# Kernel tuning notes

Measured on AMD Instinct MI355X. Metric: run time of the kernel, lower is better.

The kernel has to match this reference:

```python
import jax, jax.numpy as jnp
import numpy as np

N = 10000      # num nodes
D = 256        # embedding dim (in_channels)
Q = 4096       # num query edges
P = 0.003      # edge density (~30 avg degree)


def setup_inputs() -> dict:
    key = jax.random.key(0)
    k1, k2, k3 = jax.random.split(key, 3)
    emb_weight = jax.random.normal(k1, (N, D), dtype=jnp.float32)
    # 0/1 dense adjacency standing in for the SparseTensor adj
    adj = (jax.random.uniform(k2, (N, N)) < P).astype(jnp.float32)
    edges = jax.random.randint(k3, (2, Q), 0, N, dtype=jnp.int64)
    return {"emb_weight": emb_weight, "adj": adj, "edges": edges}


def reference(emb_weight, adj, edges):
    # model_type='simplecos', x=None -> x = emb.weight
    x = emb_weight
    degrees = adj.sum(-1) + 1e-6                      # [N]
    # x = x + (adj @ x) / degrees[:, None]  (torch precedence: matmul then div)
    x = x + (adj @ x) / degrees[:, None]              # [N, D]
    # cosine_similarity with eps=1e-8 (torch default)
    nrm = jnp.sqrt(jnp.sum(x * x, axis=1))            # [N]
    xn = x / jnp.maximum(nrm, 1e-8)[:, None]          # [N, D]
    # common neighbors: elementwise product of adjacency rows of the two endpoints
    src, dst = edges[0], edges[1]
    cn = adj[src] * adj[dst]                          # [Q, N]
    mask = (cn != 0).astype(x.dtype)                  # [Q, N] indicator of common neighbor
    # cos(x[src[e]], x[c]) and cos(x[dst[e]], x[c]) for every candidate neighbor c
    cosL = xn[src] @ xn.T                             # [Q, N]
    cosR = xn[dst] @ xn.T                             # [Q, N]
    # sparse segment-sum over common-neighbor columns
    weights = jnp.sum(mask * cosL * cosR, axis=1)     # [Q]
    return jax.nn.sigmoid(weights)
```

## Files before the change

### kernel.cpp

```cpp
#include <hip/hip_runtime.h>
#include <math.h>

#define NN 10000
#define DD 256
#define QQ 4096
#define CAP 128

typedef float  fx4 __attribute__((ext_vector_type(4)));


__global__ __launch_bounds__(256) void scan_rows(
    const float* __restrict__ adj, int* __restrict__ cnt, int* __restrict__ nbr)
{
    const int i = blockIdx.x;
    const int t = threadIdx.x;
    __shared__ int s_cnt;
    __shared__ int s_list[CAP];
    if (t == 0) s_cnt = 0;
    __syncthreads();

    const fx4* row = (const fx4*)(adj + (size_t)i * NN);
    fx4 r[10];
    #pragma unroll
    for (int j = 0; j < 10; ++j) {
        int k = t + j * 256;
        if (k < NN / 4) r[j] = __builtin_nontemporal_load(&row[k]);
        else            r[j] = (fx4){0.f, 0.f, 0.f, 0.f};
    }
    #pragma unroll
    for (int j = 0; j < 10; ++j) {
        fx4 v = r[j];
        int base = (t + j * 256) * 4;
        if (v.x != 0.f) { int p = atomicAdd(&s_cnt, 1); if (p < CAP) s_list[p] = base;     }
        if (v.y != 0.f) { int p = atomicAdd(&s_cnt, 1); if (p < CAP) s_list[p] = base + 1; }
        if (v.z != 0.f) { int p = atomicAdd(&s_cnt, 1); if (p < CAP) s_list[p] = base + 2; }
        if (v.w != 0.f) { int p = atomicAdd(&s_cnt, 1); if (p < CAP) s_list[p] = base + 3; }
    }
    __syncthreads();

    const int c = s_cnt;
    if (t == 0) cnt[i] = c;
    const int m = (c < CAP) ? c : CAP;
    if (t < m) nbr[(size_t)i * CAP + t] = s_list[t];
}

__global__ __launch_bounds__(256) void gather_rows(
    const float* __restrict__ emb, const int* __restrict__ cnt,
    const int* __restrict__ nbr, float* __restrict__ xn)
{
    const int i = blockIdx.x;
    const int t = threadIdx.x;
    __shared__ int   s_list[CAP];
    __shared__ float s_red[4];
    __shared__ float s_norm;

    const int c = cnt[i];
    const int m = (c < CAP) ? c : CAP;

    const float self = emb[(size_t)i * DD + t];
    if (t < m) s_list[t] = nbr[(size_t)i * CAP + t];
    __syncthreads();

    float a0=0.f,a1=0.f,a2=0.f,a3=0.f,a4=0.f,a5=0.f,a6=0.f,a7=0.f;
    int k = 0;
    for (; k + 8 <= m; k += 8) {
        int i0=s_list[k],   i1=s_list[k+1], i2=s_list[k+2], i3=s_list[k+3];
        int i4=s_list[k+4], i5=s_list[k+5], i6=s_list[k+6], i7=s_list[k+7];
        a0 += emb[(size_t)i0*DD + t]; a1 += emb[(size_t)i1*DD + t];
        a2 += emb[(size_t)i2*DD + t]; a3 += emb[(size_t)i3*DD + t];
        a4 += emb[(size_t)i4*DD + t]; a5 += emb[(size_t)i5*DD + t];
        a6 += emb[(size_t)i6*DD + t]; a7 += emb[(size_t)i7*DD + t];
    }
    for (; k < m; ++k) a0 += emb[(size_t)s_list[k]*DD + t];
    const float acc = ((a0+a1)+(a2+a3)) + ((a4+a5)+(a6+a7));

    const float deg = (float)c + 1e-6f;
    const float x = self + acc / deg;

    float s = x * x;
    #pragma unroll
    for (int o = 32; o > 0; o >>= 1) s += __shfl_down(s, o, 64);
    const int lane = t & 63, wv = t >> 6;
    if (lane == 0) s_red[wv] = s;
    __syncthreads();
    if (t == 0) {
        float tot = s_red[0] + s_red[1] + s_red[2] + s_red[3];
        s_norm = fmaxf(sqrtf(tot), 1e-8f);
    }
    __syncthreads();

    xn[(size_t)i * DD + t] = x / s_norm;
}

__global__ __launch_bounds__(64) void edge_weights(
    const int* __restrict__ edges, const float* __restrict__ xn,
    const int* __restrict__ cnt, const int* __restrict__ nbr,
    float* __restrict__ out)
{
    const int e = blockIdx.x;
    const int lane = threadIdx.x;
    const int srcI = edges[e];
    const int dstI = edges[QQ + e];

    __shared__ int s_dst[CAP];
    __shared__ int s_com[CAP];
    __shared__ int s_ncom;

    const int2 sA = ((const int2*)(nbr + (size_t)srcI * CAP))[lane];
    const int2 dA = ((const int2*)(nbr + (size_t)dstI * CAP))[lane];
    const int cs0 = cnt[srcI];
    const int cd0 = cnt[dstI];
    const int cs = (cs0 < CAP) ? cs0 : CAP;
    const int cd = (cd0 < CAP) ? cd0 : CAP;

    if (lane == 0) s_ncom = 0;
    s_dst[2 * lane]     = dA.x;
    s_dst[2 * lane + 1] = dA.y;
    __syncthreads();

    {
        int k0 = 2 * lane, k1 = 2 * lane + 1;
        if (k0 < cs) {
            bool f = false;
            for (int j = 0; j < cd; ++j) { if (s_dst[j] == sA.x) { f = true; break; } }
            if (f) { int p = atomicAdd(&s_ncom, 1); s_com[p] = sA.x; }
        }
        if (k1 < cs) {
            bool f = false;
            for (int j = 0; j < cd; ++j) { if (s_dst[j] == sA.y) { f = true; break; } }
            if (f) { int p = atomicAdd(&s_ncom, 1); s_com[p] = sA.y; }
        }
    }
    __syncthreads();

    const int nc = s_ncom;
    if (nc == 0) { if (lane == 0) out[e] = 0.5f; return; }

    const float4 vs = ((const float4*)(xn + (size_t)srcI * DD))[lane];
    const float4 vd = ((const float4*)(xn + (size_t)dstI * DD))[lane];

    float w = 0.f;
    for (int q = 0; q < nc; ++q) {
        const float4 vc = ((const float4*)(xn + (size_t)s_com[q] * DD))[lane];
        float a = vs.x*vc.x + vs.y*vc.y + vs.z*vc.z + vs.w*vc.w;
        float b = vd.x*vc.x + vd.y*vc.y + vd.z*vc.z + vd.w*vc.w;
        #pragma unroll
        for (int o = 32; o > 0; o >>= 1) {
            a += __shfl_xor(a, o, 64);
            b += __shfl_xor(b, o, 64);
        }
        w += a * b;
    }
    if (lane == 0) out[e] = 1.f / (1.f + expf(-w));
}

extern "C" void kernel_launch(void* const* d_in, const int* in_sizes, int n_in,
                              void* d_out, int out_size, void* d_ws, size_t ws_size,
                              hipStream_t stream) {
    const float* emb   = (const float*)d_in[0];
    const float* adj   = (const float*)d_in[1];
    const int*   edges = (const int*)d_in[2];
    float*       out   = (float*)d_out;

    float* xn  = (float*)d_ws;
    int*   cnt = (int*)(xn + (size_t)NN * DD);
    int*   nbr = cnt + NN;

    scan_rows<<<NN, 256, 0, stream>>>(adj, cnt, nbr);
    gather_rows<<<NN, 256, 0, stream>>>(emb, cnt, nbr, xn);
    edge_weights<<<QQ, 64, 0, stream>>>(edges, xn, cnt, nbr, out);
}
```

Measured before the change: 532.6 us.

## Scan adjacency rows per wave with ballot compaction and persistent grid

Measured after the change: 537.4 us. Within noise of the previous version (+0.9%).

```diff
diff --git a/kernel.cpp b/kernel.cpp
--- a/kernel.cpp
+++ b/kernel.cpp
@@ -12,36 +12,54 @@
 __global__ __launch_bounds__(256) void scan_rows(
     const float* __restrict__ adj, int* __restrict__ cnt, int* __restrict__ nbr)
 {
-    const int i = blockIdx.x;
-    const int t = threadIdx.x;
-    __shared__ int s_cnt;
-    __shared__ int s_list[CAP];
-    if (t == 0) s_cnt = 0;
-    __syncthreads();
+    const int lane = threadIdx.x & 63;
+    const int wid  = (blockIdx.x << 2) | (threadIdx.x >> 6);
+    const int nw   = gridDim.x << 2;
+    const unsigned long long lmask = (1ull << lane) - 1ull;
 
-    const fx4* row = (const fx4*)(adj + (size_t)i * NN);
-    fx4 r[10];
-    #pragma unroll
-    for (int j = 0; j < 10; ++j) {
-        int k = t + j * 256;
-        if (k < NN / 4) r[j] = __builtin_nontemporal_load(&row[k]);
-        else            r[j] = (fx4){0.f, 0.f, 0.f, 0.f};
+    for (int row = wid; row < NN; row += nw) {
+        const fx4* rp  = (const fx4*)(adj + (size_t)row * NN);
+        int* outp = nbr + (size_t)row * CAP;
+        int base = 0;
+
+        fx4 b0 = __builtin_nontemporal_load(&rp[lane]);
+        fx4 b1 = __builtin_nontemporal_load(&rp[64  + lane]);
+        fx4 b2 = __builtin_nontemporal_load(&rp[128 + lane]);
+        fx4 b3 = __builtin_nontemporal_load(&rp[192 + lane]);
+
+        #define CKCOMP(val, col)                                                  \
+            { unsigned long long _b = __ballot((val) != 0.f);                     \
+              if ((val) != 0.f) {                                                 \
+                  int _p = base + (int)__popcll(_b & lmask);                      \
+                  if (_p < CAP) outp[_p] = (col);                                 \
+              }                                                                   \
+              base += (int)__popcll(_b); }
+
+        #define CKCHUNK(v, cidx)                                                  \
+            { int _cb = (cidx) * 256 + lane * 4;                                  \
+              CKCOMP(v.x, _cb); CKCOMP(v.y, _cb + 1);                             \
+              CKCOMP(v.z, _cb + 2); CKCOMP(v.w, _cb + 3); }
+
+        for (int cc = 0; cc < 40; cc += 4) {
+            fx4 v0 = b0, v1 = b1, v2 = b2, v3 = b3;
+            int n0 = (cc + 4) * 64 + lane;
+            int n1 = (cc + 5) * 64 + lane;
+            int n2 = (cc + 6) * 64 + lane;
+            int n3 = (cc + 7) * 64 + lane;
+            b0 = (n0 < 2500) ? __builtin_nontemporal_load(&rp[n0]) : (fx4){0.f,0.f,0.f,0.f};
+            b1 = (n1 < 2500) ? __builtin_nontemporal_load(&rp[n1]) : (fx4){0.f,0.f,0.f,0.f};
+            b2 = (n2 < 2500) ? __builtin_nontemporal_load(&rp[n2]) : (fx4){0.f,0.f,0.f,0.f};
+            b3 = (n3 < 2500) ? __builtin_nontemporal_load(&rp[n3]) : (fx4){0.f,0.f,0.f,0.f};
+            CKCHUNK(v0, cc);
+            CKCHUNK(v1, cc + 1);
+            CKCHUNK(v2, cc + 2);
+            CKCHUNK(v3, cc + 3);
+        }
+        #undef CKCHUNK
+        #undef CKCOMP
+
+        if (lane == 0) cnt[row] = base;
     }
-    #pragma unroll
-    for (int j = 0; j < 10; ++j) {
-        fx4 v = r[j];
-        int base = (t + j * 256) * 4;
-        if (v.x != 0.f) { int p = atomicAdd(&s_cnt, 1); if (p < CAP) s_list[p] = base;     }
-        if (v.y != 0.f) { int p = atomicAdd(&s_cnt, 1); if (p < CAP) s_list[p] = base + 1; }
-        if (v.z != 0.f) { int p = atomicAdd(&s_cnt, 1); if (p < CAP) s_list[p] = base + 2; }
-        if (v.w != 0.f) { int p = atomicAdd(&s_cnt, 1); if (p < CAP) s_list[p] = base + 3; }
-    }
-    __syncthreads();
-
-    const int c = s_cnt;
-    if (t == 0) cnt[i] = c;
-    const int m = (c < CAP) ? c : CAP;
-    if (t < m) nbr[(size_t)i * CAP + t] = s_list[t];
 }
 
 __global__ __launch_bounds__(256) void gather_rows(
@@ -166,7 +184,7 @@
     int*   cnt = (int*)(xn + (size_t)NN * DD);
     int*   nbr = cnt + NN;
 
-    scan_rows<<<NN, 256, 0, stream>>>(adj, cnt, nbr);
+    scan_rows<<<1024, 256, 0, stream>>>(adj, cnt, nbr);
     gather_rows<<<NN, 256, 0, stream>>>(emb, cnt, nbr, xn);
     edge_weights<<<QQ, 64, 0, stream>>>(edges, xn, cnt, nbr, out);
 }
```

## Scan adjacency with flat grid-stride loop and global atomics per row

Applied to the files above, without the earlier changes.

Result: slower. 575.4 us (+8.0%).

```diff
diff --git a/kernel.cpp b/kernel.cpp
--- a/kernel.cpp
+++ b/kernel.cpp
@@ -5,43 +5,51 @@
 #define DD 256
 #define QQ 4096
 #define CAP 128
+#define FX4_PER_ROW 2500
+#define FX4_TOT     25000000
 
 typedef float  fx4 __attribute__((ext_vector_type(4)));
 
 
-__global__ __launch_bounds__(256) void scan_rows(
+__global__ __launch_bounds__(256) void zero_cnt(int* __restrict__ cnt)
+{
+    const int i = blockIdx.x * 256 + threadIdx.x;
+    if (i < NN) cnt[i] = 0;
+}
+
+__global__ __launch_bounds__(256) void scan_flat(
     const float* __restrict__ adj, int* __restrict__ cnt, int* __restrict__ nbr)
 {
-    const int i = blockIdx.x;
-    const int t = threadIdx.x;
-    __shared__ int s_cnt;
-    __shared__ int s_list[CAP];
-    if (t == 0) s_cnt = 0;
-    __syncthreads();
+    const int tid    = blockIdx.x * 256 + threadIdx.x;
+    const int stride = gridDim.x * 256;
+    const fx4* A = (const fx4*)adj;
 
-    const fx4* row = (const fx4*)(adj + (size_t)i * NN);
-    fx4 r[10];
-    #pragma unroll
-    for (int j = 0; j < 10; ++j) {
-        int k = t + j * 256;
-        if (k < NN / 4) r[j] = __builtin_nontemporal_load(&row[k]);
-        else            r[j] = (fx4){0.f, 0.f, 0.f, 0.f};
+    #define PROC(v, k)                                                        \
+        if (v.x != 0.f || v.y != 0.f || v.z != 0.f || v.w != 0.f) {           \
+            int _row = (k) / FX4_PER_ROW;                                     \
+            int _cb  = ((k) - _row * FX4_PER_ROW) * 4;                        \
+            if (v.x != 0.f) { int p = atomicAdd(&cnt[_row], 1); if (p < CAP) nbr[_row * CAP + p] = _cb;     } \
+            if (v.y != 0.f) { int p = atomicAdd(&cnt[_row], 1); if (p < CAP) nbr[_row * CAP + p] = _cb + 1; } \
+            if (v.z != 0.f) { int p = atomicAdd(&cnt[_row], 1); if (p < CAP) nbr[_row * CAP + p] = _cb + 2; } \
+            if (v.w != 0.f) { int p = atomicAdd(&cnt[_row], 1); if (p < CAP) nbr[_row * CAP + p] = _cb + 3; } \
+        }
+
+    int k = tid;
+    for (; k + 3 * stride < FX4_TOT; k += 4 * stride) {
+        fx4 v0 = A[k];
+        fx4 v1 = A[k + stride];
+        fx4 v2 = A[k + 2 * stride];
+        fx4 v3 = A[k + 3 * stride];
+        PROC(v0, k);
+        PROC(v1, k + stride);
+        PROC(v2, k + 2 * stride);
+        PROC(v3, k + 3 * stride);
     }
-    #pragma unroll
-    for (int j = 0; j < 10; ++j) {
-        fx4 v = r[j];
-        int base = (t + j * 256) * 4;
-        if (v.x != 0.f) { int p = atomicAdd(&s_cnt, 1); if (p < CAP) s_list[p] = base;     }
-        if (v.y != 0.f) { int p = atomicAdd(&s_cnt, 1); if (p < CAP) s_list[p] = base + 1; }
-        if (v.z != 0.f) { int p = atomicAdd(&s_cnt, 1); if (p < CAP) s_list[p] = base + 2; }
-        if (v.w != 0.f) { int p = atomicAdd(&s_cnt, 1); if (p < CAP) s_list[p] = base + 3; }
+    for (; k < FX4_TOT; k += stride) {
+        fx4 v = A[k];
+        PROC(v, k);
     }
-    __syncthreads();
-
-    const int c = s_cnt;
-    if (t == 0) cnt[i] = c;
-    const int m = (c < CAP) ? c : CAP;
-    if (t < m) nbr[(size_t)i * CAP + t] = s_list[t];
+    #undef PROC
 }
 
 __global__ __launch_bounds__(256) void gather_rows(
@@ -166,7 +174,8 @@
     int*   cnt = (int*)(xn + (size_t)NN * DD);
     int*   nbr = cnt + NN;
 
-    scan_rows<<<NN, 256, 0, stream>>>(adj, cnt, nbr);
+    zero_cnt<<<40, 256, 0, stream>>>(cnt);
+    scan_flat<<<2048, 256, 0, stream>>>(adj, cnt, nbr);
     gather_rows<<<NN, 256, 0, stream>>>(emb, cnt, nbr, xn);
     edge_weights<<<QQ, 64, 0, stream>>>(edges, xn, cnt, nbr, out);
 }
```
